# Performance work log

Hardware: AMD Instinct MI355X
Metric: run time of the kernel (lower is better)

Reference implementation:

```python
import jax, jax.numpy as jnp
import numpy as np

B, N, C = 8, 4096, 1024
H = 16
D = C // H  # head_dim = 64
SCALE = D ** -0.5


def setup_inputs() -> dict:
    key = jax.random.key(0)
    ks = jax.random.split(key, 5)
    std = C ** -0.5
    return {
        "x": jax.random.normal(ks[0], (B, N, C), dtype=jnp.float32),
        "Wq": jax.random.normal(ks[1], (C, C), dtype=jnp.float32) * std,
        "Wk": jax.random.normal(ks[2], (C, C), dtype=jnp.float32) * std,
        "Wv": jax.random.normal(ks[3], (C, C), dtype=jnp.float32) * std,
        "Wo": jax.random.normal(ks[4], (C, C), dtype=jnp.float32) * std,
        "bo": jnp.zeros((C,), dtype=jnp.float32),
    }


def reference(x, Wq, Wk, Wv, Wo, bo):
    b, n, c = x.shape
    # projections -> (B, N, H, D)
    q = (x @ Wq).reshape(b, n, H, D)
    k = (x @ Wk).reshape(b, n, H, D)
    v = (x @ Wv).reshape(b, n, H, D)
    # feature maps: softmax over head_dim for q, over sequence for k
    q = jax.nn.softmax(q, axis=-1) * SCALE
    k = jax.nn.softmax(k, axis=1)
    # O(N) linear attention: kv summary then apply to q
    kv = jnp.einsum("bnhf,bnhd->bhfd", k, v)   # (B, H, D, D)
    y = jnp.einsum("bnhf,bhfd->bnhd", q, kv)   # (B, N, H, D)
    y = y.reshape(b, n, H * D)
    return y @ Wo + bo
```

## Files before the change

kernel.cpp:

```cpp
#include <hip/hip_runtime.h>


typedef unsigned short u16;
typedef __bf16 bf16x8v __attribute__((ext_vector_type(8)));
typedef float f32x4 __attribute__((ext_vector_type(4)));
typedef u16 u16x8 __attribute__((ext_vector_type(8)));
typedef u16 u16x4 __attribute__((ext_vector_type(4)));

#define AS1C(p) (const __attribute__((address_space(1))) void*)(p)
#define AS3(p)  (__attribute__((address_space(3))) void*)(p)

__device__ __forceinline__ float b2f(u16 u) {
    union { unsigned u; float f; } c; c.u = ((unsigned)u) << 16; return c.f;
}
__device__ __forceinline__ u16 f2b(float f) {
    union { float f; unsigned u; } c; c.f = f;
    unsigned x = c.u + 0x7fffu + ((c.u >> 16) & 1u);
    return (u16)(x >> 16);
}

__global__ void prep(const float* __restrict__ x, u16* __restrict__ xb,
                     const float* __restrict__ Wq, const float* __restrict__ Wk,
                     const float* __restrict__ Wv, const float* __restrict__ Wo,
                     u16* __restrict__ wt, u16* __restrict__ wot) {
    if (blockIdx.x < 1024) {
        __shared__ float tl[64][65];
        const int which = blockIdx.x >> 8;
        const float* src = which == 0 ? Wq : which == 1 ? Wk : which == 2 ? Wv : Wo;
        u16* dst = which < 3 ? wt + which * 1048576 : wot;
        const int bx = blockIdx.x & 255;
        const int tx = bx & 15, ty = bx >> 4;
        const int j = threadIdx.x & 63, i0 = threadIdx.x >> 6;
        #pragma unroll
        for (int it = 0; it < 16; ++it) {
            int i = it * 4 + i0;
            tl[i][j] = src[(ty * 64 + i) * 1024 + tx * 64 + j];
        }
        __syncthreads();
        #pragma unroll
        for (int it = 0; it < 16; ++it) {
            int i = it * 4 + i0;
            dst[(tx * 64 + i) * 1024 + ty * 64 + j] = f2b(tl[j][i]);
        }
    } else {
        const long n4 = 8388608L;
        long i = (long)(blockIdx.x - 1024) * blockDim.x + threadIdx.x;
        long stride = 2048L * blockDim.x;
        for (long jj = i; jj < n4; jj += stride) {
            float4 v = ((const float4*)x)[jj];
            u16x4 o = { f2b(v.x), f2b(v.y), f2b(v.z), f2b(v.w) };
            ((u16x4*)xb)[jj] = o;
        }
    }
}

template<int OUTMODE>
__global__ __launch_bounds__(512, 2) void gemm256(
    const u16* __restrict__ A, const u16* __restrict__ Bt,
    void* __restrict__ Cout, const float* __restrict__ bias,
    const int lda, const int ldc, const int ntn, const int nwg)
{
    __shared__ __align__(16) u16 lds[65536];
    const int t = threadIdx.x;
    const int w = t >> 6, lane = t & 63;
    const int l16 = lane & 15, g = lane >> 4;
    const int wr = w >> 2, wc = w & 3;

    const int cpx = nwg >> 3;
    const int bid = blockIdx.x;
    const int swzb = (bid & 7) * cpx + (bid >> 3);
    const int tm = swzb / ntn, tn = swzb - tm * ntn;
    const long row0 = (long)tm << 8, col0 = (long)tn << 8;

    const int eo = (((t & 7) ^ ((t >> 3) & 7)) << 3);
    const u16* pA = A + (row0 + (t >> 3)) * (long)lda + eo;
    const u16* pB = Bt + (col0 + (t >> 3)) * 1024L + eo;
    const long a64 = (long)lda << 6;

#define STG_A(Tt, j) __builtin_amdgcn_global_load_lds(                        \
    AS1C(pA + (long)(j) * a64 + (((Tt) & 15) << 6)),                          \
    AS3(lds + ((((Tt) & 1) << 15) + ((j) << 12) + t * 8)), 16, 0, 0);
#define STG_B(Tt, j) __builtin_amdgcn_global_load_lds(                        \
    AS1C(pB + (long)(j) * 65536L + (((Tt) & 15) << 6)),                       \
    AS3(lds + ((((Tt) & 1) << 15) + 16384 + ((j) << 12) + t * 8)), 16, 0, 0);

    const int swz = l16 & 7;
    const int koff0 = ((0 * 4 + g) ^ swz) << 3;
    const int koff1 = ((1 * 4 + g) ^ swz) << 3;
    const int arow = ((wr << 7) + l16) << 6;
    const int brow = 16384 + (((wc << 6) + l16) << 6);

    u16x8 aM[4][2], b0[2][2], b1[2][2];
    f32x4 acc[8][4] = {};

#define RD_A(half) { _Pragma("unroll") for (int mi = 0; mi < 4; ++mi) {       \
    const int ab = bufE + arow + ((half) * 64 + mi * 16) * 64;                \
    aM[mi][0] = *(const u16x8*)&lds[ab + koff0];                              \
    aM[mi][1] = *(const u16x8*)&lds[ab + koff1]; } }
#define RD_B(nh, br) { _Pragma("unroll") for (int ni = 0; ni < 2; ++ni) {     \
    const int bb = bufE + brow + ((nh) * 32 + ni * 16) * 64;                  \
    br[ni][0] = *(const u16x8*)&lds[bb + koff0];                              \
    br[ni][1] = *(const u16x8*)&lds[bb + koff1]; } }
#define MM(mh, nh, br) { __builtin_amdgcn_s_setprio(1);                       \
    _Pragma("unroll") for (int mi = 0; mi < 4; ++mi)                          \
    { _Pragma("unroll") for (int ni = 0; ni < 2; ++ni) {                      \
    f32x4 c = acc[(mh)*4 + mi][(nh)*2 + ni];                                  \
    c = __builtin_amdgcn_mfma_f32_16x16x32_bf16(                              \
        __builtin_bit_cast(bf16x8v, aM[mi][0]),                               \
        __builtin_bit_cast(bf16x8v, br[ni][0]), c, 0, 0, 0);                  \
    c = __builtin_amdgcn_mfma_f32_16x16x32_bf16(                              \
        __builtin_bit_cast(bf16x8v, aM[mi][1]),                               \
        __builtin_bit_cast(bf16x8v, br[ni][1]), c, 0, 0, 0);                  \
    acc[(mh)*4 + mi][(nh)*2 + ni] = c; } }                                    \
    __builtin_amdgcn_s_setprio(0); }

    STG_A(0, 0) STG_A(0, 2) STG_B(0, 0) STG_B(0, 1)
    STG_B(0, 2) STG_B(0, 3) STG_A(0, 1) STG_A(0, 3)
    STG_A(1, 0) STG_A(1, 2) STG_B(1, 0) STG_B(1, 1)
    asm volatile("s_waitcnt vmcnt(6)" ::: "memory");
    __builtin_amdgcn_s_barrier();

    #pragma unroll 2
    for (int T = 0; T < 16; ++T) {
        const int bufE = (T & 1) << 15;
        RD_A(0) RD_B(0, b0)
        STG_B(T + 1, 2) STG_B(T + 1, 3)
        __builtin_amdgcn_s_barrier();
        MM(0, 0, b0)
        RD_B(1, b1)
        STG_A(T + 1, 1) STG_A(T + 1, 3)
        asm volatile("s_waitcnt vmcnt(8)" ::: "memory");
        __builtin_amdgcn_s_barrier();
        MM(0, 1, b1)
        RD_A(1)
        STG_A(T + 2, 0) STG_A(T + 2, 2)
        __builtin_amdgcn_s_barrier();
        MM(1, 0, b0)
        STG_B(T + 2, 0) STG_B(T + 2, 1)
        asm volatile("s_waitcnt vmcnt(6)" ::: "memory");
        __builtin_amdgcn_s_barrier();
        MM(1, 1, b1)
    }
    asm volatile("s_waitcnt vmcnt(0)" ::: "memory");
#undef STG_A
#undef STG_B
#undef RD_A
#undef RD_B
#undef MM

    if (OUTMODE == 2 && tn < 4) {
        #pragma unroll
        for (int mi = 0; mi < 8; ++mi) {
            #pragma unroll
            for (int r = 0; r < 4; ++r) {
                float v0 = acc[mi][0][r], v1 = acc[mi][1][r];
                float v2 = acc[mi][2][r], v3 = acc[mi][3][r];
                float m = fmaxf(fmaxf(v0, v1), fmaxf(v2, v3));
                m = fmaxf(m, __shfl_xor(m, 1)); m = fmaxf(m, __shfl_xor(m, 2));
                m = fmaxf(m, __shfl_xor(m, 4)); m = fmaxf(m, __shfl_xor(m, 8));
                v0 = __expf(v0 - m); v1 = __expf(v1 - m);
                v2 = __expf(v2 - m); v3 = __expf(v3 - m);
                float s = v0 + v1 + v2 + v3;
                s += __shfl_xor(s, 1); s += __shfl_xor(s, 2);
                s += __shfl_xor(s, 4); s += __shfl_xor(s, 8);
                const float sc = 0.125f / s;
                acc[mi][0][r] = v0 * sc; acc[mi][1][r] = v1 * sc;
                acc[mi][2][r] = v2 * sc; acc[mi][3][r] = v3 * sc;
            }
        }
    }

    const long crow = row0 + wr * 128 + g * 4;
    const long ccol = col0 + wc * 64 + l16;
    if (OUTMODE != 1) {
        u16* Cb = (u16*)Cout;
        #pragma unroll
        for (int mi = 0; mi < 8; ++mi) {
            #pragma unroll
            for (int ni = 0; ni < 4; ++ni) {
                long base = (crow + mi * 16) * (long)ldc + ccol + ni * 16;
                #pragma unroll
                for (int r = 0; r < 4; ++r)
                    Cb[base + (long)r * ldc] = f2b(acc[mi][ni][r]);
            }
        }
    } else {
        float* Cf = (float*)Cout;
        float bv[4];
        #pragma unroll
        for (int ni = 0; ni < 4; ++ni) bv[ni] = bias[ccol + ni * 16];
        #pragma unroll
        for (int mi = 0; mi < 8; ++mi) {
            #pragma unroll
            for (int ni = 0; ni < 4; ++ni) {
                long base = (crow + mi * 16) * (long)ldc + ccol + ni * 16;
                #pragma unroll
                for (int r = 0; r < 4; ++r)
                    Cf[base + (long)r * ldc] = acc[mi][ni][r] + bv[ni];
            }
        }
    }
}

__global__ __launch_bounds__(256) void kv_partial(const u16* __restrict__ qkv,
                                                  float* __restrict__ kvp,
                                                  float* __restrict__ psum) {
    __shared__ __align__(16) float kf_s[64 * 68];
    __shared__ __align__(16) float v_s[64 * 68];
    const int t = threadIdx.x;
    const int bx = blockIdx.x;
    const int nc = bx & 7, h = (bx >> 3) & 15, b = bx >> 7;
    const int f0 = (t >> 4) << 2;
    const int d0 = (t & 15) << 2;
    const int lr = t >> 3, lc = (t & 7) << 3;
    const long rowbase = (long)b * 4096 + nc * 512;
    const u16* kfg = qkv + (rowbase + lr) * 3072 + 1024 + h * 64 + lc;
    const u16* vg = kfg + 1024;
    float acc[4][4] = {};
    float cs[4] = {};
    for (int n0 = 0; n0 < 512; n0 += 64) {
        long go = (long)n0 * 3072;
        u16x8 kr0 = *(const u16x8*)(kfg + go);
        u16x8 kr1 = *(const u16x8*)(kfg + go + 32L * 3072);
        u16x8 vr0 = *(const u16x8*)(vg + go);
        u16x8 vr1 = *(const u16x8*)(vg + go + 32L * 3072);
        f32x4 ke0a, ke0b, ke1a, ke1b, vv0a, vv0b, vv1a, vv1b;
        #pragma unroll
        for (int j = 0; j < 4; ++j) {
            ke0a[j] = __expf(b2f(kr0[j]));     ke0b[j] = __expf(b2f(kr0[j + 4]));
            ke1a[j] = __expf(b2f(kr1[j]));     ke1b[j] = __expf(b2f(kr1[j + 4]));
            vv0a[j] = b2f(vr0[j]);             vv0b[j] = b2f(vr0[j + 4]);
            vv1a[j] = b2f(vr1[j]);             vv1b[j] = b2f(vr1[j + 4]);
        }
        *(f32x4*)&kf_s[lr * 68 + lc]            = ke0a;
        *(f32x4*)&kf_s[lr * 68 + lc + 4]        = ke0b;
        *(f32x4*)&kf_s[(lr + 32) * 68 + lc]     = ke1a;
        *(f32x4*)&kf_s[(lr + 32) * 68 + lc + 4] = ke1b;
        *(f32x4*)&v_s[lr * 68 + lc]             = vv0a;
        *(f32x4*)&v_s[lr * 68 + lc + 4]         = vv0b;
        *(f32x4*)&v_s[(lr + 32) * 68 + lc]      = vv1a;
        *(f32x4*)&v_s[(lr + 32) * 68 + lc + 4]  = vv1b;
        __syncthreads();
        #pragma unroll 8
        for (int r = 0; r < 64; ++r) {
            f32x4 kf4 = *(const f32x4*)&kf_s[r * 68 + f0];
            f32x4 vf4 = *(const f32x4*)&v_s[r * 68 + d0];
            #pragma unroll
            for (int i = 0; i < 4; ++i) {
                cs[i] += kf4[i];
                #pragma unroll
                for (int jj = 0; jj < 4; ++jj)
                    acc[i][jj] += kf4[i] * vf4[jj];
            }
        }
        __syncthreads();
    }
    float* o = kvp + (long)nc * 524288 + ((long)(b * 16 + h)) * 4096;
    #pragma unroll
    for (int i = 0; i < 4; ++i) {
        #pragma unroll
        for (int jj = 0; jj < 4; ++jj)
            o[(f0 + i) * 64 + d0 + jj] = acc[i][jj];
    }
    if ((t & 15) == 0) {
        float* ps = psum + ((long)nc * 128 + b * 16 + h) * 64 + f0;
        #pragma unroll
        for (int i = 0; i < 4; ++i) ps[i] = cs[i];
    }
}

__global__ void kv_combine_T(const float* __restrict__ kvp, const float* __restrict__ psum,
                             u16* __restrict__ kvTb) {
    __shared__ float tl[64 * 65];
    __shared__ float inv_s[64];
    const int bh = blockIdx.x;
    const int t = threadIdx.x;
    if (t < 64) {
        float s = 0.f;
        #pragma unroll
        for (int nc = 0; nc < 8; ++nc) s += psum[((long)nc * 128 + bh) * 64 + t];
        inv_s[t] = 1.0f / s;
    }
    __syncthreads();
    const float* p = kvp + (long)bh * 4096;
    #pragma unroll
    for (int it = 0; it < 16; ++it) {
        int idx = it * 256 + t;
        float v = 0.f;
        #pragma unroll
        for (int nc = 0; nc < 8; ++nc) v += p[(long)nc * 524288 + idx];
        tl[(idx & 63) * 65 + (idx >> 6)] = v * inv_s[idx >> 6];
    }
    __syncthreads();
    u16* o = kvTb + (long)bh * 4096;
    #pragma unroll
    for (int it = 0; it < 16; ++it) {
        int idx = it * 256 + t;
        o[idx] = f2b(tl[(idx >> 6) * 65 + (idx & 63)]);
    }
}

__global__ __launch_bounds__(256) void apply_mfma(u16* __restrict__ qkv,
                                                  const u16* __restrict__ kvTb) {
    __shared__ __align__(16) u16 Qs[8192];
    const int t = threadIdx.x;
    const int bx = blockIdx.x;
    const int nt = bx & 31, h = (bx >> 5) & 15, b = bx >> 9;
    const long n0 = (long)b * 4096 + (long)nt * 128;
    const int wave = t >> 6, lane = t & 63;
    const int wr = wave >> 1, wc = wave & 1;
    const int l16 = lane & 15, g = lane >> 4;

    const int colg = t & 7;
    const int rloc = t >> 3;
    #pragma unroll
    for (int p = 0; p < 4; ++p) {
        const int row = p * 32 + rloc;
        u16x8 qv = *(const u16x8*)(qkv + (n0 + row) * 3072 + h * 64 + colg * 8);
        const int chunk = colg ^ (row & 7);
        *(u16x8*)&Qs[row * 64 + chunk * 8] = qv;
    }
    __syncthreads();

    const u16* kvb = kvTb + ((long)(b * 16 + h) << 12);
    bf16x8v bkv[2][2];
    #pragma unroll
    for (int ni = 0; ni < 2; ++ni) {
        #pragma unroll
        for (int ks = 0; ks < 2; ++ks)
            bkv[ni][ks] = __builtin_bit_cast(bf16x8v,
                *(const u16x8*)(kvb + (wc * 32 + ni * 16 + l16) * 64 + ks * 32 + g * 8));
    }
    bf16x8v aq[4][2];
    #pragma unroll
    for (int mi = 0; mi < 4; ++mi) {
        const int row = wr * 64 + mi * 16 + l16;
        #pragma unroll
        for (int ks = 0; ks < 2; ++ks) {
            const int c16 = (ks * 4 + g) ^ (row & 7);
            aq[mi][ks] = __builtin_bit_cast(bf16x8v,
                *(const u16x8*)&Qs[row * 64 + c16 * 8]);
        }
    }
    f32x4 acc[4][2] = {};
    #pragma unroll
    for (int mi = 0; mi < 4; ++mi) {
        #pragma unroll
        for (int ni = 0; ni < 2; ++ni) {
            acc[mi][ni] = __builtin_amdgcn_mfma_f32_16x16x32_bf16(
                aq[mi][0], bkv[ni][0], acc[mi][ni], 0, 0, 0);
            acc[mi][ni] = __builtin_amdgcn_mfma_f32_16x16x32_bf16(
                aq[mi][1], bkv[ni][1], acc[mi][ni], 0, 0, 0);
        }
    }
    #pragma unroll
    for (int mi = 0; mi < 4; ++mi) {
        #pragma unroll
        for (int ni = 0; ni < 2; ++ni) {
            long row = n0 + wr * 64 + mi * 16 + g * 4;
            int col = h * 64 + wc * 32 + ni * 16 + l16;
            #pragma unroll
            for (int r = 0; r < 4; ++r)
                qkv[(row + r) * 3072 + col] = f2b(acc[mi][ni][r]);
        }
    }
}

extern "C" void kernel_launch(void* const* d_in, const int* in_sizes, int n_in,
                              void* d_out, int out_size, void* d_ws, size_t ws_size,
                              hipStream_t stream) {
    (void)in_sizes; (void)n_in; (void)out_size; (void)ws_size;
    const float* x  = (const float*)d_in[0];
    const float* Wq = (const float*)d_in[1];
    const float* Wk = (const float*)d_in[2];
    const float* Wv = (const float*)d_in[3];
    const float* Wo = (const float*)d_in[4];
    const float* bo = (const float*)d_in[5];

    u16* xb  = (u16*)d_ws;
    u16* wt  = xb + 33554432;
    u16* wot = wt + 3145728;
    u16* qkv = wot + 1048576;
    u16*   kvTb = qkv + 100663296;
    float* kvp  = (float*)xb;
    float* psum = kvp + 4194304;

    prep<<<3072, 256, 0, stream>>>(x, xb, Wq, Wk, Wv, Wo, wt, wot);
    gemm256<2><<<1536, 512, 0, stream>>>(xb, wt, (void*)qkv, nullptr, 1024, 3072, 12, 1536);
    kv_partial<<<1024, 256, 0, stream>>>(qkv, kvp, psum);
    kv_combine_T<<<128, 256, 0, stream>>>(kvp, psum, kvTb);
    apply_mfma<<<4096, 256, 0, stream>>>(qkv, kvTb);
    gemm256<1><<<512, 512, 0, stream>>>(qkv, wot, d_out, bo, 3072, 1024, 4, 512);
}
```

Before: 417.2 us.

## Fold per-batch KV summary into output weights instead of applying to Q

Reassociates y@Wo = q·(kv·Wo_h). A small per-batch MFMA kernel premultiplies each head's normalized kv into the output projection weights, and the final GEMM then reads the softmaxed Q directly with a batch-indexed B operand. This removes the apply pass, which read and wrote the whole Q region. The exp for the K feature map also moves out of kv_partial into the QKV GEMM epilogue. The cost is a per-batch weight matrix (8x1024x1024 bf16) that adds global memory traffic and changes bf16 rounding points.

```diff
diff --git a/kernel.cpp b/kernel.cpp
--- a/kernel.cpp
+++ b/kernel.cpp
@@ -58,7 +58,7 @@
 __global__ __launch_bounds__(512, 2) void gemm256(
     const u16* __restrict__ A, const u16* __restrict__ Bt,
     void* __restrict__ Cout, const float* __restrict__ bias,
-    const int lda, const int ldc, const int ntn, const int nwg)
+    const int lda, const int ldc, const int ntn, const int nwg, const long btBatch)
 {
     __shared__ __align__(16) u16 lds[65536];
     const int t = threadIdx.x;
@@ -71,10 +71,11 @@
     const int swzb = (bid & 7) * cpx + (bid >> 3);
     const int tm = swzb / ntn, tn = swzb - tm * ntn;
     const long row0 = (long)tm << 8, col0 = (long)tn << 8;
+    const u16* BtB = Bt + (row0 >> 12) * btBatch;
 
     const int eo = (((t & 7) ^ ((t >> 3) & 7)) << 3);
     const u16* pA = A + (row0 + (t >> 3)) * (long)lda + eo;
-    const u16* pB = Bt + (col0 + (t >> 3)) * 1024L + eo;
+    const u16* pB = BtB + (col0 + (t >> 3)) * 1024L + eo;
     const long a64 = (long)lda << 6;
 
 #define STG_A(Tt, j) __builtin_amdgcn_global_load_lds(                        \
@@ -168,6 +169,15 @@
                 acc[mi][2][r] = v2 * sc; acc[mi][3][r] = v3 * sc;
             }
         }
+    }
+    if (OUTMODE == 2 && tn >= 4 && tn < 8) {
+        #pragma unroll
+        for (int mi = 0; mi < 8; ++mi)
+            #pragma unroll
+            for (int ni = 0; ni < 4; ++ni)
+                #pragma unroll
+                for (int r = 0; r < 4; ++r)
+                    acc[mi][ni][r] = __expf(acc[mi][ni][r]);
     }
 
     const long crow = row0 + wr * 128 + g * 4;
@@ -227,10 +237,10 @@
         f32x4 ke0a, ke0b, ke1a, ke1b, vv0a, vv0b, vv1a, vv1b;
         #pragma unroll
         for (int j = 0; j < 4; ++j) {
-            ke0a[j] = __expf(b2f(kr0[j]));     ke0b[j] = __expf(b2f(kr0[j + 4]));
-            ke1a[j] = __expf(b2f(kr1[j]));     ke1b[j] = __expf(b2f(kr1[j + 4]));
-            vv0a[j] = b2f(vr0[j]);             vv0b[j] = b2f(vr0[j + 4]);
-            vv1a[j] = b2f(vr1[j]);             vv1b[j] = b2f(vr1[j + 4]);
+            ke0a[j] = b2f(kr0[j]);     ke0b[j] = b2f(kr0[j + 4]);
+            ke1a[j] = b2f(kr1[j]);     ke1b[j] = b2f(kr1[j + 4]);
+            vv0a[j] = b2f(vr0[j]);     vv0b[j] = b2f(vr0[j + 4]);
+            vv1a[j] = b2f(vr1[j]);     vv1b[j] = b2f(vr1[j + 4]);
         }
         *(f32x4*)&kf_s[lr * 68 + lc]            = ke0a;
         *(f32x4*)&kf_s[lr * 68 + lc + 4]        = ke0b;
@@ -269,9 +279,8 @@
     }
 }
 
-__global__ void kv_combine_T(const float* __restrict__ kvp, const float* __restrict__ psum,
-                             u16* __restrict__ kvTb) {
-    __shared__ float tl[64 * 65];
+__global__ void kv_scale(const float* __restrict__ kvp, const float* __restrict__ psum,
+                         u16* __restrict__ kvNb) {
     __shared__ float inv_s[64];
     const int bh = blockIdx.x;
     const int t = threadIdx.x;
@@ -283,30 +292,31 @@
     }
     __syncthreads();
     const float* p = kvp + (long)bh * 4096;
-    #pragma unroll
-    for (int it = 0; it < 16; ++it) {
-        int idx = it * 256 + t;
-        float v = 0.f;
-        #pragma unroll
-        for (int nc = 0; nc < 8; ++nc) v += p[(long)nc * 524288 + idx];
-        tl[(idx & 63) * 65 + (idx >> 6)] = v * inv_s[idx >> 6];
-    }
-    __syncthreads();
-    u16* o = kvTb + (long)bh * 4096;
-    #pragma unroll
-    for (int it = 0; it < 16; ++it) {
-        int idx = it * 256 + t;
-        o[idx] = f2b(tl[(idx >> 6) * 65 + (idx & 63)]);
-    }
-}
-
-__global__ __launch_bounds__(256) void apply_mfma(u16* __restrict__ qkv,
-                                                  const u16* __restrict__ kvTb) {
+    u16* o = kvNb + (long)bh * 4096;
+    const float inv = inv_s[t >> 2];
+    #pragma unroll
+    for (int j = 0; j < 4; ++j) {
+        const int idx = t * 16 + j * 4;
+        f32x4 v = {};
+        #pragma unroll
+        for (int nc = 0; nc < 8; ++nc) {
+            f32x4 pv = *(const f32x4*)&p[(long)nc * 524288 + idx];
+            #pragma unroll
+            for (int e = 0; e < 4; ++e) v[e] += pv[e];
+        }
+        u16x4 ov = { f2b(v[0] * inv), f2b(v[1] * inv), f2b(v[2] * inv), f2b(v[3] * inv) };
+        *(u16x4*)&o[idx] = ov;
+    }
+}
+
+__global__ __launch_bounds__(256) void w2t_mfma(const u16* __restrict__ wot,
+                                                const u16* __restrict__ kvNb,
+                                                u16* __restrict__ w2t) {
     __shared__ __align__(16) u16 Qs[8192];
     const int t = threadIdx.x;
     const int bx = blockIdx.x;
-    const int nt = bx & 31, h = (bx >> 5) & 15, b = bx >> 9;
-    const long n0 = (long)b * 4096 + (long)nt * 128;
+    const int mt = bx & 7, h = (bx >> 3) & 15, b = bx >> 7;
+    const int c0 = mt * 128;
     const int wave = t >> 6, lane = t & 63;
     const int wr = wave >> 1, wc = wave & 1;
     const int l16 = lane & 15, g = lane >> 4;
@@ -316,13 +326,13 @@
     #pragma unroll
     for (int p = 0; p < 4; ++p) {
         const int row = p * 32 + rloc;
-        u16x8 qv = *(const u16x8*)(qkv + (n0 + row) * 3072 + h * 64 + colg * 8);
+        u16x8 qv = *(const u16x8*)(wot + (long)(c0 + row) * 1024 + h * 64 + colg * 8);
         const int chunk = colg ^ (row & 7);
         *(u16x8*)&Qs[row * 64 + chunk * 8] = qv;
     }
     __syncthreads();
 
-    const u16* kvb = kvTb + ((long)(b * 16 + h) << 12);
+    const u16* kvb = kvNb + ((long)(b * 16 + h) << 12);
     bf16x8v bkv[2][2];
     #pragma unroll
     for (int ni = 0; ni < 2; ++ni) {
@@ -353,15 +363,16 @@
                 aq[mi][1], bkv[ni][1], acc[mi][ni], 0, 0, 0);
         }
     }
+    u16* ob = w2t + (long)b * 1048576;
     #pragma unroll
     for (int mi = 0; mi < 4; ++mi) {
         #pragma unroll
         for (int ni = 0; ni < 2; ++ni) {
-            long row = n0 + wr * 64 + mi * 16 + g * 4;
+            int row = c0 + wr * 64 + mi * 16 + g * 4;
             int col = h * 64 + wc * 32 + ni * 16 + l16;
             #pragma unroll
             for (int r = 0; r < 4; ++r)
-                qkv[(row + r) * 3072 + col] = f2b(acc[mi][ni][r]);
+                ob[(long)(row + r) * 1024 + col] = f2b(acc[mi][ni][r]);
         }
     }
 }
@@ -381,14 +392,15 @@
     u16* wt  = xb + 33554432;
     u16* wot = wt + 3145728;
     u16* qkv = wot + 1048576;
-    u16*   kvTb = qkv + 100663296;
+    u16* kvNb = qkv + 100663296;
     float* kvp  = (float*)xb;
     float* psum = kvp + 4194304;
+    u16* w2t = (u16*)(psum + 65536);
 
     prep<<<3072, 256, 0, stream>>>(x, xb, Wq, Wk, Wv, Wo, wt, wot);
-    gemm256<2><<<1536, 512, 0, stream>>>(xb, wt, (void*)qkv, nullptr, 1024, 3072, 12, 1536);
+    gemm256<2><<<1536, 512, 0, stream>>>(xb, wt, (void*)qkv, nullptr, 1024, 3072, 12, 1536, 0L);
     kv_partial<<<1024, 256, 0, stream>>>(qkv, kvp, psum);
-    kv_combine_T<<<128, 256, 0, stream>>>(kvp, psum, kvTb);
-    apply_mfma<<<4096, 256, 0, stream>>>(qkv, kvTb);
-    gemm256<1><<<512, 512, 0, stream>>>(qkv, wot, d_out, bo, 3072, 1024, 4, 512);
-}
+    kv_scale<<<128, 256, 0, stream>>>(kvp, psum, kvNb);
+    w2t_mfma<<<1024, 256, 0, stream>>>(wot, kvNb, w2t);
+    gemm256<1><<<512, 512, 0, stream>>>(qkv, w2t, d_out, bo, 3072, 1024, 4, 512, 1048576L);
+}
```

New measurement: 385.4 us. 1.08x faster.
